# Kernel tuning notes

Hardware: AMD Instinct MI355X
Metric: run time of the kernel (lower is better)

Reference implementation:

```python
import jax, jax.numpy as jnp
import numpy as np
import math

HIDDEN = 128   # hidden_size (per-head dim) used for 1/sqrt(d) scaling
SPAN = 1024    # attn_span
B, M = 32, 1024
K_LEN = M + SPAN


def _unskew(X, span):
    """X: [B, M, K] -> [B, M, span], out[b,m,l] = X[b, m, m+l].
    Equivalent to the torch pad/view/slice trick (shift row m left by m)."""
    _, Mq, _ = X.shape
    rows = jnp.arange(Mq)[:, None]                 # [M,1]
    cols = rows + jnp.arange(span)[None, :]        # [M,span]
    return X[:, rows, cols]


def _skew(X, pad_value):
    """X: [B, M, L] -> [B, M, M+L], out[b,m,j] = X[b,m,j-m] if 0<=j-m<L else pad.
    Equivalent to the torch pad/view/slice trick (shift row m right by m)."""
    _, Mq, L = X.shape
    m = jnp.arange(Mq)[:, None]                    # [M,1]
    rel = jnp.arange(Mq + L)[None, :] - m          # [M, M+L]
    valid = (rel >= 0) & (rel < L)
    gathered = X[:, m, jnp.clip(rel, 0, L - 1)]    # [B, M, M+L]
    return jnp.where(valid, gathered, pad_value)


def setup_inputs() -> dict:
    key = jax.random.key(0)
    k1, k2, k3, k4 = jax.random.split(key, 4)
    return {
        "query": jax.random.normal(k1, (B, M, HIDDEN), dtype=jnp.float32),
        "key": jax.random.normal(k2, (B, K_LEN, HIDDEN), dtype=jnp.float32),
        "value": jax.random.normal(k3, (B, K_LEN, HIDDEN), dtype=jnp.float32),
        "pos_encoding": jax.random.normal(k4, (HIDDEN, SPAN), dtype=jnp.float32),
    }


def reference(query, key, value, pos_encoding):
    span = pos_encoding.shape[-1]
    # context scores: [B, M, M+span]
    attn_ctx = jnp.einsum('bmh,bkh->bmk', query, key)
    attn_ctx = _unskew(attn_ctx, span)             # [B, M, span]
    # relative-position scores: [B, M, span]
    attn_pos = jnp.einsum('bmh,hl->bml', query, pos_encoding)
    attn = (attn_ctx + attn_pos) / math.sqrt(HIDDEN)
    attn = jax.nn.softmax(attn, axis=-1)           # dropout p=0 -> identity
    attn_sk = _skew(attn, 0.0)                     # [B, M, M+span]
    return jnp.einsum('bmk,bkh->bmh', attn_sk, value)
```

## Files before the change

kernel.cpp:

```cpp
#include <hip/hip_runtime.h>
#include <hip/hip_bf16.h>

#define B_    32
#define M_    1024
#define H_    128
#define SPAN_ 1024
#define KL_   2048
#define NITER 17
#define SCALE 0.08838834764831845f

typedef __attribute__((ext_vector_type(8))) short bf16x8;
typedef __attribute__((ext_vector_type(4))) float f32x4;

#define WSNEED 262144ull

static __device__ __forceinline__ unsigned int cvt_pk2(float lo, float hi) {
  unsigned int r;
  asm("v_cvt_pk_bf16_f32 %0, %1, %2" : "=v"(r) : "v"(lo), "v"(hi));
  return r;
}
static __device__ __forceinline__ unsigned short f2b(float x) {
  unsigned int u = __builtin_bit_cast(unsigned int, x);
  return (unsigned short)((u + 0x7FFFu + ((u >> 16) & 1u)) >> 16);
}
static __device__ __forceinline__ float b2f(unsigned short u) {
  return __builtin_bit_cast(float, ((unsigned int)u) << 16);
}
static __device__ __forceinline__ bf16x8 ldfrag(const char* p) {
  short4 a = *(const short4*)p;
  short4 b = *(const short4*)(p + 8);
  bf16x8 r;
  r[0] = a.x; r[1] = a.y; r[2] = a.z; r[3] = a.w;
  r[4] = b.x; r[5] = b.y; r[6] = b.z; r[7] = b.w;
  return r;
}

__global__ void __launch_bounds__(256) convP2(const float* __restrict__ pe,
                                              char* __restrict__ out) {
  __shared__ float tile[128 * 66];
  int lt = blockIdx.x, tid = threadIdx.x;
#pragma unroll
  for (int i = 0; i < 8; ++i) {
    int idx = i * 256 + tid;
    int h = idx >> 4, c4 = idx & 15;
    float4 x = *(const float4*)(pe + (size_t)h * 1024 + lt * 64 + c4 * 4);
    tile[h * 66 + c4 * 4 + 0] = x.x; tile[h * 66 + c4 * 4 + 1] = x.y;
    tile[h * 66 + c4 * 4 + 2] = x.z; tile[h * 66 + c4 * 4 + 3] = x.w;
  }
  __syncthreads();
  char* dst = out + (size_t)lt * 16384;
#pragma unroll
  for (int j = 0; j < 4; ++j) {
    int u = tid >> 4;
    int l = (tid & 15) + 16 * j;
    uint4 d;
    d.x = cvt_pk2(tile[(8 * u + 0) * 66 + l], tile[(8 * u + 1) * 66 + l]);
    d.y = cvt_pk2(tile[(8 * u + 2) * 66 + l], tile[(8 * u + 3) * 66 + l]);
    d.z = cvt_pk2(tile[(8 * u + 4) * 66 + l], tile[(8 * u + 5) * 66 + l]);
    d.w = cvt_pk2(tile[(8 * u + 6) * 66 + l], tile[(8 * u + 7) * 66 + l]);
    *(uint4*)(dst + l * 256 + 16 * u) = d;
  }
}

#define PITCH_A  264
#define PITCH_VT 136
#define PITCH_PR 264
#define PITCH_PW 136
#define OFF_K  0
#define OFF_VT 16896
#define OFF_PT 34304
#define OFF_PR 51200
#define OFF_PW 68096
#define LDS_FB 76800

__global__ void __launch_bounds__(256, 2) seqattn_main(
    const float* __restrict__ q, const float* __restrict__ kkey,
    const float* __restrict__ vval, const char* __restrict__ posws,
    float* __restrict__ out) {
  extern __shared__ char smem[];
  char* KL = smem + OFF_K;
  char* VT = smem + OFF_VT;
  char* PT = smem + OFF_PT;
  char* PR = smem + OFF_PR;
  char* PW = smem + OFF_PW;

  int jb = blockIdx.x;
  int o  = (jb & 7) * 64 + (jb >> 3);
  int b  = o >> 4;
  int m0 = (o & 15) * 64;

  int tid  = threadIdx.x;
  int w    = tid >> 6;
  int lane = tid & 63;
  int g    = lane >> 4;
  int c    = lane & 15;
  int r0   = tid >> 5;
  int c4   = tid & 31;

  const float* qbase = q    + ((size_t)b * M_  + m0) * H_;
  const float* kbase = kkey + ((size_t)b * KL_ + m0) * H_;
  const float* vbase = vval + ((size_t)b * KL_ + m0) * H_;

  float4 kpre[8];
  float  vpre[32];
  uint4  ppre[4];

#define LOADK(tt) do {                                                        \
    const float* kb_ = kbase + (size_t)(64 * (tt)) * H_;                      \
    _Pragma("unroll")                                                         \
    for (int p = 0; p < 8; ++p)                                               \
      kpre[p] = *(const float4*)(kb_ + (p * 8 + r0) * H_ + c4 * 4);           \
  } while (0)
#define WRITEK() do {                                                         \
    _Pragma("unroll")                                                         \
    for (int p = 0; p < 8; ++p) {                                             \
      float4 v_ = kpre[p];                                                    \
      uint2 d_; d_.x = cvt_pk2(v_.x, v_.y); d_.y = cvt_pk2(v_.z, v_.w);       \
      *(uint2*)(KL + (p * 8 + r0) * PITCH_A + c4 * 8) = d_;                   \
    }                                                                         \
  } while (0)
#define LOADV(tt) do {                                                        \
    const float* vb_ = vbase + (size_t)(64 * (tt)) * H_;                      \
    _Pragma("unroll")                                                         \
    for (int qq = 0; qq < 4; ++qq) {                                          \
      int kq_ = 4 * (4 * w + qq);                                             \
      _Pragma("unroll")                                                       \
      for (int r = 0; r < 4; ++r) {                                           \
        vpre[qq * 8 + r * 2 + 0] = vb_[(kq_ + r) * H_ + lane];                \
        vpre[qq * 8 + r * 2 + 1] = vb_[(kq_ + r) * H_ + lane + 64];           \
      }                                                                       \
    }                                                                         \
  } while (0)
#define WRITEV() do {                                                         \
    _Pragma("unroll")                                                         \
    for (int qq = 0; qq < 4; ++qq) {                                          \
      int kq_ = 4 * w + qq;                                                   \
      uint2 lo_, hi_;                                                         \
      lo_.x = cvt_pk2(vpre[qq * 8 + 0], vpre[qq * 8 + 2]);                    \
      lo_.y = cvt_pk2(vpre[qq * 8 + 4], vpre[qq * 8 + 6]);                    \
      hi_.x = cvt_pk2(vpre[qq * 8 + 1], vpre[qq * 8 + 3]);                    \
      hi_.y = cvt_pk2(vpre[qq * 8 + 5], vpre[qq * 8 + 7]);                    \
      *(uint2*)(VT + lane * PITCH_VT + 8 * kq_) = lo_;                        \
      *(uint2*)(VT + (lane + 64) * PITCH_VT + 8 * kq_) = hi_;                 \
    }                                                                         \
  } while (0)
#define LOADP2(tt) do {                                                       \
    const char* pt_ = posws + (size_t)(tt) * 16384;                           \
    _Pragma("unroll")                                                         \
    for (int i = 0; i < 4; ++i)                                               \
      ppre[i] = *(const uint4*)(pt_ + (i * 256 + tid) * 16);                  \
  } while (0)
#define WRITEP2() do {                                                        \
    _Pragma("unroll")                                                         \
    for (int i = 0; i < 4; ++i) {                                             \
      int idx_ = i * 256 + tid;                                               \
      int pr_ = idx_ >> 4, pu_ = idx_ & 15;                                   \
      uint2 lo_, hi_;                                                         \
      lo_.x = ppre[i].x; lo_.y = ppre[i].y;                                   \
      hi_.x = ppre[i].z; hi_.y = ppre[i].w;                                   \
      *(uint2*)(PT + pr_ * PITCH_A + pu_ * 16) = lo_;                         \
      *(uint2*)(PT + pr_ * PITCH_A + pu_ * 16 + 8) = hi_;                     \
    }                                                                         \
  } while (0)

  {
    float4 qpre[8];
#pragma unroll
    for (int p = 0; p < 8; ++p)
      qpre[p] = *(const float4*)(qbase + (p * 8 + r0) * H_ + c4 * 4);
    LOADK(0); LOADV(0); LOADP2(0);
#pragma unroll
    for (int p = 0; p < 8; ++p) {
      float4 v_ = qpre[p];
      uint2 d_;
      d_.x = cvt_pk2(v_.x * SCALE, v_.y * SCALE);
      d_.y = cvt_pk2(v_.z * SCALE, v_.w * SCALE);
      *(uint2*)(PR + (p * 8 + r0) * PITCH_PR + c4 * 8) = d_;
    }
    WRITEK(); WRITEV(); WRITEP2();
    LOADK(1); LOADV(1); LOADP2(1);
  }
  __syncthreads();

  bf16x8 qf[4];
#pragma unroll
  for (int hs = 0; hs < 4; ++hs)
    qf[hs] = ldfrag(PR + (w * 16 + c) * PITCH_PR + hs * 64 + g * 16);

  f32x4 O[8];
#pragma unroll
  for (int i = 0; i < 8; ++i) { O[i][0] = 0.f; O[i][1] = 0.f; O[i][2] = 0.f; O[i][3] = 0.f; }
  float mrun = -1e30f, lrun = 0.f;
  const int mrow = 16 * w + c;
  char* prRow = PR + mrow * PITCH_PR;
  char* pwRow = PW + mrow * PITCH_PW;

#pragma unroll 1
  for (int t = 0; t < NITER; ++t) {
    if (t < 16) {
      __builtin_amdgcn_s_setprio(1);
#pragma unroll
      for (int lt = 0; lt < 4; ++lt) {
        f32x4 pb = {0.f, 0.f, 0.f, 0.f};
#pragma unroll
        for (int hs = 0; hs < 4; ++hs)
          pb = __builtin_amdgcn_mfma_f32_16x16x32_bf16(
              ldfrag(PT + (16 * lt + c) * PITCH_A + hs * 64 + g * 16), qf[hs], pb, 0, 0, 0);
#pragma unroll
        for (int rr = 0; rr < 4; ++rr) {
          int x = (64 * t + 16 * lt + 4 * g + rr + mrow) & 127;
          *(unsigned short*)(prRow + x * 2) = f2b(pb[rr]);
        }
      }
      __builtin_amdgcn_s_setprio(0);
    }
    f32x4 s[4];
    __builtin_amdgcn_s_setprio(1);
#pragma unroll
    for (int nt = 0; nt < 4; ++nt) {
      f32x4 acc = {0.f, 0.f, 0.f, 0.f};
#pragma unroll
      for (int hs = 0; hs < 4; ++hs)
        acc = __builtin_amdgcn_mfma_f32_16x16x32_bf16(
            ldfrag(KL + (16 * nt + c) * PITCH_A + hs * 64 + g * 16), qf[hs], acc, 0, 0, 0);
      s[nt] = acc;
    }
    __builtin_amdgcn_s_setprio(0);
#pragma unroll
    for (int nt = 0; nt < 4; ++nt) {
      int x = (64 * t + 16 * nt + 4 * g) & 127;
      ushort4 bv = *(const ushort4*)(prRow + x * 2);
      int lbase = 64 * t + 16 * nt + 4 * g - mrow;
      const unsigned short* bp = (const unsigned short*)&bv;
#pragma unroll
      for (int rr = 0; rr < 4; ++rr) {
        float sv = s[nt][rr] + b2f(bp[rr]);
        s[nt][rr] = ((unsigned)(lbase + rr) < 1024u) ? sv : -1e30f;
      }
    }
    float pmax = -1e30f;
#pragma unroll
    for (int nt = 0; nt < 4; ++nt)
#pragma unroll
      for (int rr = 0; rr < 4; ++rr) pmax = fmaxf(pmax, s[nt][rr]);
    pmax = fmaxf(pmax, __shfl_xor(pmax, 16, 64));
    pmax = fmaxf(pmax, __shfl_xor(pmax, 32, 64));
    if (__any(pmax > mrun + 8.0f)) {
      float mn = fmaxf(mrun, pmax);
      float corr = __expf(mrun - mn);
      mrun = mn;
      lrun *= corr;
#pragma unroll
      for (int i = 0; i < 8; ++i) {
        O[i][0] *= corr; O[i][1] *= corr; O[i][2] *= corr; O[i][3] *= corr;
      }
    }
    float rsum = 0.f;
#pragma unroll
    for (int nt = 0; nt < 4; ++nt) {
      float p0 = __expf(s[nt][0] - mrun);
      float p1 = __expf(s[nt][1] - mrun);
      float p2 = __expf(s[nt][2] - mrun);
      float p3 = __expf(s[nt][3] - mrun);
      rsum += (p0 + p1) + (p2 + p3);
      uint2 d_;
      d_.x = cvt_pk2(p0, p1);
      d_.y = cvt_pk2(p2, p3);
      *(uint2*)(pwRow + (16 * nt + 4 * g) * 2) = d_;
    }
    rsum += __shfl_xor(rsum, 16, 64);
    rsum += __shfl_xor(rsum, 32, 64);
    lrun += rsum;
    __builtin_amdgcn_s_setprio(1);
#pragma unroll
    for (int ks = 0; ks < 2; ++ks) {
      bf16x8 pfrag = ldfrag(pwRow + ks * 64 + g * 16);
#pragma unroll
      for (int nt = 0; nt < 8; ++nt)
        O[nt] = __builtin_amdgcn_mfma_f32_16x16x32_bf16(
            ldfrag(VT + (16 * nt + c) * PITCH_VT + ks * 64 + g * 16), pfrag, O[nt], 0, 0, 0);
    }
    __builtin_amdgcn_s_setprio(0);
    __syncthreads();
    if (t < 16) {
      WRITEK(); WRITEV();
      if (t < 15) {
        WRITEP2();
        LOADK(t + 2); LOADV(t + 2);
        if (t + 2 < 16) LOADP2(t + 2);
      }
    }
    __syncthreads();
  }

  float inv = 1.0f / lrun;
  float* ob = out + ((size_t)b * M_ + m0 + mrow) * H_;
#pragma unroll
  for (int nt = 0; nt < 8; ++nt) {
    float4 vv;
    vv.x = O[nt][0] * inv; vv.y = O[nt][1] * inv;
    vv.z = O[nt][2] * inv; vv.w = O[nt][3] * inv;
    *(float4*)(ob + 16 * nt + 4 * g) = vv;
  }
}
#undef LOADK
#undef WRITEK
#undef LOADV
#undef WRITEV
#undef LOADP2
#undef WRITEP2

__global__ void __launch_bounds__(256, 2) seqattn_fb(
    const float* __restrict__ q, const float* __restrict__ kkey,
    const float* __restrict__ vval, const float* __restrict__ pe,
    float* __restrict__ out) {
  extern __shared__ char smem[];
  char* KL = smem + OFF_K;
  char* VT = smem + OFF_VT;
  char* PT = smem + OFF_PT;
  char* PR = smem + OFF_PR;
  char* PW = smem + OFF_PW;

  int jb = blockIdx.x;
  int o  = (jb & 7) * 64 + (jb >> 3);
  int b  = o >> 4;
  int m0 = (o & 15) * 64;

  int tid  = threadIdx.x;
  int w    = tid >> 6;
  int lane = tid & 63;
  int g    = lane >> 4;
  int c    = lane & 15;
  int r0   = tid >> 5;
  int c4   = tid & 31;

  const float* qbase = q    + ((size_t)b * M_  + m0) * H_;
  const float* kbase = kkey + ((size_t)b * KL_ + m0) * H_;
  const float* vbase = vval + ((size_t)b * KL_ + m0) * H_;

  float4 kpre[8];
  float  vpre[32];
  float  ppre[32];

#define LOADK(tt) do {                                                        \
    const float* kb_ = kbase + (size_t)(64 * (tt)) * H_;                      \
    _Pragma("unroll")                                                         \
    for (int p = 0; p < 8; ++p)                                               \
      kpre[p] = *(const float4*)(kb_ + (p * 8 + r0) * H_ + c4 * 4);           \
  } while (0)
#define WRITEK() do {                                                         \
    _Pragma("unroll")                                                         \
    for (int p = 0; p < 8; ++p) {                                             \
      float4 v_ = kpre[p];                                                    \
      uint2 d_; d_.x = cvt_pk2(v_.x, v_.y); d_.y = cvt_pk2(v_.z, v_.w);       \
      *(uint2*)(KL + (p * 8 + r0) * PITCH_A + c4 * 8) = d_;                   \
    }                                                                         \
  } while (0)
#define LOADV(tt) do {                                                        \
    const float* vb_ = vbase + (size_t)(64 * (tt)) * H_;                      \
    _Pragma("unroll")                                                         \
    for (int qq = 0; qq < 4; ++qq) {                                          \
      int kq_ = 4 * (4 * w + qq);                                             \
      _Pragma("unroll")                                                       \
      for (int r = 0; r < 4; ++r) {                                           \
        vpre[qq * 8 + r * 2 + 0] = vb_[(kq_ + r) * H_ + lane];                \
        vpre[qq * 8 + r * 2 + 1] = vb_[(kq_ + r) * H_ + lane + 64];           \
      }                                                                       \
    }                                                                         \
  } while (0)
#define WRITEV() do {                                                         \
    _Pragma("unroll")                                                         \
    for (int qq = 0; qq < 4; ++qq) {                                          \
      int kq_ = 4 * w + qq;                                                   \
      uint2 lo_, hi_;                                                         \
      lo_.x = cvt_pk2(vpre[qq * 8 + 0], vpre[qq * 8 + 2]);                    \
      lo_.y = cvt_pk2(vpre[qq * 8 + 4], vpre[qq * 8 + 6]);                    \
      hi_.x = cvt_pk2(vpre[qq * 8 + 1], vpre[qq * 8 + 3]);                    \
      hi_.y = cvt_pk2(vpre[qq * 8 + 5], vpre[qq * 8 + 7]);                    \
      *(uint2*)(VT + lane * PITCH_VT + 8 * kq_) = lo_;                        \
      *(uint2*)(VT + (lane + 64) * PITCH_VT + 8 * kq_) = hi_;                 \
    }                                                                         \
  } while (0)
#define LOADP(tt) do {                                                        \
    const float* pb_ = pe + 64 * (tt);                                        \
    _Pragma("unroll")                                                         \
    for (int qq = 0; qq < 8; ++qq) {                                          \
      int h_ = 4 * (8 * w + qq);                                              \
      _Pragma("unroll")                                                       \
      for (int r = 0; r < 4; ++r)                                             \
        ppre[qq * 4 + r] = pb_[(h_ + r) * SPAN_ + lane];                      \
    }                                                                         \
  } while (0)
#define WRITEP() do {                                                         \
    _Pragma("unroll")                                                         \
    for (int qq = 0; qq < 8; ++qq) {                                          \
      uint2 d_;                                                               \
      d_.x = cvt_pk2(ppre[qq * 4 + 0], ppre[qq * 4 + 1]);                     \
      d_.y = cvt_pk2(ppre[qq * 4 + 2], ppre[qq * 4 + 3]);                     \
      *(uint2*)(PT + lane * PITCH_A + 8 * (8 * w + qq)) = d_;                 \
    }                                                                         \
  } while (0)

  {
    float4 qpre[8];
#pragma unroll
    for (int p = 0; p < 8; ++p)
      qpre[p] = *(const float4*)(qbase + (p * 8 + r0) * H_ + c4 * 4);
    LOADK(0); LOADV(0); LOADP(0);
#pragma unroll
    for (int p = 0; p < 8; ++p) {
      float4 v_ = qpre[p];
      uint2 d_;
      d_.x = cvt_pk2(v_.x * SCALE, v_.y * SCALE);
      d_.y = cvt_pk2(v_.z * SCALE, v_.w * SCALE);
      *(uint2*)(PR + (p * 8 + r0) * PITCH_PR + c4 * 8) = d_;
    }
    WRITEK(); WRITEV(); WRITEP();
    LOADK(1); LOADV(1); LOADP(1);
  }
  __syncthreads();

  bf16x8 qf[4];
#pragma unroll
  for (int hs = 0; hs < 4; ++hs)
    qf[hs] = ldfrag(PR + (w * 16 + c) * PITCH_PR + hs * 64 + g * 16);

  f32x4 O[8];
#pragma unroll
  for (int i = 0; i < 8; ++i) { O[i][0] = 0.f; O[i][1] = 0.f; O[i][2] = 0.f; O[i][3] = 0.f; }
  float mrun = -1e30f, lrun = 0.f;
  const int mrow = 16 * w + c;
  char* prRow = PR + mrow * PITCH_PR;
  char* pwRow = PW + mrow * PITCH_PW;

#pragma unroll 1
  for (int t = 0; t < NITER; ++t) {
    if (t < 16) {
#pragma unroll
      for (int lt = 0; lt < 4; ++lt) {
        f32x4 pb = {0.f, 0.f, 0.f, 0.f};
#pragma unroll
        for (int hs = 0; hs < 4; ++hs)
          pb = __builtin_amdgcn_mfma_f32_16x16x32_bf16(
              ldfrag(PT + (16 * lt + c) * PITCH_A + hs * 64 + g * 16), qf[hs], pb, 0, 0, 0);
#pragma unroll
        for (int rr = 0; rr < 4; ++rr) {
          int x = (64 * t + 16 * lt + 4 * g + rr + mrow) & 127;
          *(unsigned short*)(prRow + x * 2) = f2b(pb[rr]);
        }
      }
    }
    f32x4 s[4];
#pragma unroll
    for (int nt = 0; nt < 4; ++nt) {
      f32x4 acc = {0.f, 0.f, 0.f, 0.f};
#pragma unroll
      for (int hs = 0; hs < 4; ++hs)
        acc = __builtin_amdgcn_mfma_f32_16x16x32_bf16(
            ldfrag(KL + (16 * nt + c) * PITCH_A + hs * 64 + g * 16), qf[hs], acc, 0, 0, 0);
      s[nt] = acc;
    }
#pragma unroll
    for (int nt = 0; nt < 4; ++nt) {
      int x = (64 * t + 16 * nt + 4 * g) & 127;
      ushort4 bv = *(const ushort4*)(prRow + x * 2);
      int lbase = 64 * t + 16 * nt + 4 * g - mrow;
      const unsigned short* bp = (const unsigned short*)&bv;
#pragma unroll
      for (int rr = 0; rr < 4; ++rr) {
        float sv = s[nt][rr] + b2f(bp[rr]);
        s[nt][rr] = ((unsigned)(lbase + rr) < 1024u) ? sv : -1e30f;
      }
    }
    float pmax = -1e30f;
#pragma unroll
    for (int nt = 0; nt < 4; ++nt)
#pragma unroll
      for (int rr = 0; rr < 4; ++rr) pmax = fmaxf(pmax, s[nt][rr]);
    pmax = fmaxf(pmax, __shfl_xor(pmax, 16, 64));
    pmax = fmaxf(pmax, __shfl_xor(pmax, 32, 64));
    if (__any(pmax > mrun + 8.0f)) {
      float mn = fmaxf(mrun, pmax);
      float corr = __expf(mrun - mn);
      mrun = mn;
      lrun *= corr;
#pragma unroll
      for (int i = 0; i < 8; ++i) {
        O[i][0] *= corr; O[i][1] *= corr; O[i][2] *= corr; O[i][3] *= corr;
      }
    }
    float rsum = 0.f;
#pragma unroll
    for (int nt = 0; nt < 4; ++nt) {
      float p0 = __expf(s[nt][0] - mrun);
      float p1 = __expf(s[nt][1] - mrun);
      float p2 = __expf(s[nt][2] - mrun);
      float p3 = __expf(s[nt][3] - mrun);
      rsum += (p0 + p1) + (p2 + p3);
      uint2 d_;
      d_.x = cvt_pk2(p0, p1);
      d_.y = cvt_pk2(p2, p3);
      *(uint2*)(pwRow + (16 * nt + 4 * g) * 2) = d_;
    }
    rsum += __shfl_xor(rsum, 16, 64);
    rsum += __shfl_xor(rsum, 32, 64);
    lrun += rsum;
#pragma unroll
    for (int ks = 0; ks < 2; ++ks) {
      bf16x8 pfrag = ldfrag(pwRow + ks * 64 + g * 16);
#pragma unroll
      for (int nt = 0; nt < 8; ++nt)
        O[nt] = __builtin_amdgcn_mfma_f32_16x16x32_bf16(
            ldfrag(VT + (16 * nt + c) * PITCH_VT + ks * 64 + g * 16), pfrag, O[nt], 0, 0, 0);
    }
    __syncthreads();
    if (t < 16) {
      WRITEK(); WRITEV();
      if (t < 15) {
        WRITEP();
        LOADK(t + 2); LOADV(t + 2);
        if (t + 2 < 16) LOADP(t + 2);
      }
    }
    __syncthreads();
  }

  float inv = 1.0f / lrun;
  float* ob = out + ((size_t)b * M_ + m0 + mrow) * H_;
#pragma unroll
  for (int nt = 0; nt < 8; ++nt) {
    float4 vv;
    vv.x = O[nt][0] * inv; vv.y = O[nt][1] * inv;
    vv.z = O[nt][2] * inv; vv.w = O[nt][3] * inv;
    *(float4*)(ob + 16 * nt + 4 * g) = vv;
  }
}
#undef LOADK
#undef WRITEK
#undef LOADV
#undef WRITEV
#undef LOADP
#undef WRITEP

extern "C" void kernel_launch(void* const* d_in, const int* in_sizes, int n_in,
                              void* d_out, int out_size, void* d_ws, size_t ws_size,
                              hipStream_t stream) {
  const float* q  = (const float*)d_in[0];
  const float* k  = (const float*)d_in[1];
  const float* v  = (const float*)d_in[2];
  const float* pe = (const float*)d_in[3];
  float* out = (float*)d_out;

  if (ws_size >= WSNEED) {
    char* ws = (char*)d_ws;
    convP2<<<dim3(16), dim3(256), 0, stream>>>(pe, ws);
    (void)hipFuncSetAttribute(reinterpret_cast<const void*>(seqattn_main),
                              hipFuncAttributeMaxDynamicSharedMemorySize, LDS_FB);
    seqattn_main<<<dim3(512), dim3(256), LDS_FB, stream>>>(q, k, v, ws, out);
  } else {
    (void)hipFuncSetAttribute(reinterpret_cast<const void*>(seqattn_fb),
                              hipFuncAttributeMaxDynamicSharedMemorySize, LDS_FB);
    seqattn_fb<<<dim3(512), dim3(256), LDS_FB, stream>>>(q, k, v, pe, out);
  }
}
```

Before: 80.41 us.

## Warp-specialize attention kernel with producer waves and direct global-to-LDS pos loads

Restructures the main kernel into 512-thread blocks where four waves act as producers that load and convert K/V tiles to bf16 and stage the positional tile via global_load_lds, while four consumer waves run the MFMA score, softmax and PV work. The positional workspace is now written with an XOR swizzle, so the consumer reads it directly without padding. The aim is to overlap global loads with compute and take register pressure for prefetch buffers off the compute waves. The cost is extra waves per block, two barriers per iteration and a different LDS layout, which could limit occupancy.

```diff
diff --git a/kernel.cpp b/kernel.cpp
--- a/kernel.cpp
+++ b/kernel.cpp
@@ -33,6 +33,11 @@
   r[0] = a.x; r[1] = a.y; r[2] = a.z; r[3] = a.w;
   r[4] = b.x; r[5] = b.y; r[6] = b.z; r[7] = b.w;
   return r;
+}
+static __device__ __forceinline__ void gll16(char* lds, const char* g) {
+  __builtin_amdgcn_global_load_lds(
+      (const __attribute__((address_space(1))) unsigned int*)g,
+      (__attribute__((address_space(3))) unsigned int*)lds, 16, 0, 0);
 }
 
 __global__ void __launch_bounds__(256) convP2(const float* __restrict__ pe,
@@ -58,12 +63,256 @@
     d.y = cvt_pk2(tile[(8 * u + 2) * 66 + l], tile[(8 * u + 3) * 66 + l]);
     d.z = cvt_pk2(tile[(8 * u + 4) * 66 + l], tile[(8 * u + 5) * 66 + l]);
     d.w = cvt_pk2(tile[(8 * u + 6) * 66 + l], tile[(8 * u + 7) * 66 + l]);
-    *(uint4*)(dst + l * 256 + 16 * u) = d;
+    *(uint4*)(dst + l * 256 + 16 * (u ^ (l & 7))) = d;
   }
 }
 
 #define PITCH_A  264
 #define PITCH_VT 136
+#define MOFF_K  0
+#define MOFF_VT 16896
+#define MOFF_PT 34304
+#define MOFF_PR 50688
+#define MOFF_PW 67584
+#define LDS_MAIN 76288
+
+__global__ void __launch_bounds__(512, 4) seqattn_main(
+    const float* __restrict__ q, const float* __restrict__ kkey,
+    const float* __restrict__ vval, const char* __restrict__ posws,
+    float* __restrict__ out) {
+  extern __shared__ char smem[];
+  char* KL = smem + MOFF_K;
+  char* VT = smem + MOFF_VT;
+  char* PT = smem + MOFF_PT;
+  char* PR = smem + MOFF_PR;
+  char* PW = smem + MOFF_PW;
+
+  int jb = blockIdx.x;
+  int o  = (jb & 7) * 64 + (jb >> 3);
+  int b  = o >> 4;
+  int m0 = (o & 15) * 64;
+
+  int tid  = threadIdx.x;
+  bool isProd = tid >= 256;
+  int w    = tid >> 6;
+  int lane = tid & 63;
+  int g    = lane >> 4;
+  int c    = lane & 15;
+  int r0   = tid >> 5;
+  int c4   = tid & 31;
+  int sx   = c & 7;
+  int ptid  = tid & 255;
+  int pw    = ptid >> 6;
+  int plane = ptid & 63;
+  int pr0   = ptid >> 5;
+  int pc4   = ptid & 31;
+
+  const float* qbase = q    + ((size_t)b * M_  + m0) * H_;
+  const float* kbase = kkey + ((size_t)b * KL_ + m0) * H_;
+  const float* vbase = vval + ((size_t)b * KL_ + m0) * H_;
+
+  uint2 kbf[8];
+  uint2 vlo[4], vhi[4];
+
+#define PLOADK(tt) do {                                                       \
+    const float* kb_ = kbase + (size_t)(64 * (tt)) * H_;                      \
+    _Pragma("unroll")                                                         \
+    for (int p = 0; p < 8; ++p) {                                             \
+      float4 v_ = *(const float4*)(kb_ + (p * 8 + pr0) * H_ + pc4 * 4);       \
+      kbf[p].x = cvt_pk2(v_.x, v_.y);                                         \
+      kbf[p].y = cvt_pk2(v_.z, v_.w);                                         \
+    }                                                                         \
+  } while (0)
+#define PWRITEK() do {                                                        \
+    _Pragma("unroll")                                                         \
+    for (int p = 0; p < 8; ++p)                                               \
+      *(uint2*)(KL + (p * 8 + pr0) * PITCH_A + pc4 * 8) = kbf[p];             \
+  } while (0)
+#define PLOADV(tt) do {                                                       \
+    const float* vb_ = vbase + (size_t)(64 * (tt)) * H_;                      \
+    _Pragma("unroll")                                                         \
+    for (int qq = 0; qq < 4; ++qq) {                                          \
+      int kq_ = 4 * (4 * pw + qq);                                            \
+      float a0 = vb_[(kq_ + 0) * H_ + plane];                                 \
+      float a1 = vb_[(kq_ + 1) * H_ + plane];                                 \
+      float a2 = vb_[(kq_ + 2) * H_ + plane];                                 \
+      float a3 = vb_[(kq_ + 3) * H_ + plane];                                 \
+      float b0 = vb_[(kq_ + 0) * H_ + plane + 64];                            \
+      float b1 = vb_[(kq_ + 1) * H_ + plane + 64];                            \
+      float b2 = vb_[(kq_ + 2) * H_ + plane + 64];                            \
+      float b3 = vb_[(kq_ + 3) * H_ + plane + 64];                            \
+      vlo[qq].x = cvt_pk2(a0, a1); vlo[qq].y = cvt_pk2(a2, a3);               \
+      vhi[qq].x = cvt_pk2(b0, b1); vhi[qq].y = cvt_pk2(b2, b3);               \
+    }                                                                         \
+  } while (0)
+#define PWRITEV() do {                                                        \
+    _Pragma("unroll")                                                         \
+    for (int qq = 0; qq < 4; ++qq) {                                          \
+      int kq_ = 4 * pw + qq;                                                  \
+      *(uint2*)(VT + plane * PITCH_VT + 8 * kq_) = vlo[qq];                   \
+      *(uint2*)(VT + (plane + 64) * PITCH_VT + 8 * kq_) = vhi[qq];            \
+    }                                                                         \
+  } while (0)
+#define PSTAGEP(tt) do {                                                      \
+    const char* ps_ = posws + (size_t)(tt) * 16384;                           \
+    _Pragma("unroll")                                                         \
+    for (int i = 0; i < 4; ++i)                                               \
+      gll16(PT + (4 * pw + i) * 1024, ps_ + (4 * pw + i) * 1024 + plane * 16);\
+  } while (0)
+
+  if (!isProd) {
+    float4 qpre[8];
+#pragma unroll
+    for (int p = 0; p < 8; ++p)
+      qpre[p] = *(const float4*)(qbase + (p * 8 + r0) * H_ + c4 * 4);
+#pragma unroll
+    for (int p = 0; p < 8; ++p) {
+      float4 v_ = qpre[p];
+      uint2 d_;
+      d_.x = cvt_pk2(v_.x * SCALE, v_.y * SCALE);
+      d_.y = cvt_pk2(v_.z * SCALE, v_.w * SCALE);
+      *(uint2*)(PR + (p * 8 + r0) * PITCH_A + c4 * 8) = d_;
+    }
+  } else {
+    PLOADK(0); PLOADV(0);
+    PSTAGEP(0);
+    PWRITEK(); PWRITEV();
+  }
+  __syncthreads();
+
+  bf16x8 qf[4];
+  if (!isProd) {
+#pragma unroll
+    for (int hs = 0; hs < 4; ++hs)
+      qf[hs] = ldfrag(PR + (w * 16 + c) * PITCH_A + hs * 64 + g * 16);
+  }
+
+  f32x4 O[8];
+#pragma unroll
+  for (int i = 0; i < 8; ++i) { O[i][0] = 0.f; O[i][1] = 0.f; O[i][2] = 0.f; O[i][3] = 0.f; }
+  float mrun = -1e30f, lrun = 0.f;
+  const int mrow = 16 * w + c;
+  char* prRow = PR + mrow * PITCH_A;
+  char* pwRow = PW + mrow * PITCH_VT;
+
+#pragma unroll 1
+  for (int t = 0; t < NITER; ++t) {
+    if (!isProd) {
+      if (t < 16) {
+        __builtin_amdgcn_s_setprio(1);
+#pragma unroll
+        for (int lt = 0; lt < 4; ++lt) {
+          f32x4 pb = {0.f, 0.f, 0.f, 0.f};
+#pragma unroll
+          for (int hs = 0; hs < 4; ++hs) {
+            const char* pp = PT + (16 * lt + c) * 256 + 16 * (((hs << 2) | g) ^ sx);
+            pb = __builtin_amdgcn_mfma_f32_16x16x32_bf16(
+                *(const bf16x8*)pp, qf[hs], pb, 0, 0, 0);
+          }
+#pragma unroll
+          for (int rr = 0; rr < 4; ++rr) {
+            int x = (64 * t + 16 * lt + 4 * g + rr + mrow) & 127;
+            *(unsigned short*)(prRow + x * 2) = f2b(pb[rr]);
+          }
+        }
+        __builtin_amdgcn_s_setprio(0);
+      }
+      f32x4 s[4];
+      __builtin_amdgcn_s_setprio(1);
+#pragma unroll
+      for (int nt = 0; nt < 4; ++nt) {
+        f32x4 acc = {0.f, 0.f, 0.f, 0.f};
+#pragma unroll
+        for (int hs = 0; hs < 4; ++hs)
+          acc = __builtin_amdgcn_mfma_f32_16x16x32_bf16(
+              ldfrag(KL + (16 * nt + c) * PITCH_A + hs * 64 + g * 16), qf[hs], acc, 0, 0, 0);
+        s[nt] = acc;
+      }
+      __builtin_amdgcn_s_setprio(0);
+#pragma unroll
+      for (int nt = 0; nt < 4; ++nt) {
+        int x = (64 * t + 16 * nt + 4 * g) & 127;
+        ushort4 bv = *(const ushort4*)(prRow + x * 2);
+        int lbase = 64 * t + 16 * nt + 4 * g - mrow;
+        const unsigned short* bp = (const unsigned short*)&bv;
+#pragma unroll
+        for (int rr = 0; rr < 4; ++rr) {
+          float sv = s[nt][rr] + b2f(bp[rr]);
+          s[nt][rr] = ((unsigned)(lbase + rr) < 1024u) ? sv : -1e30f;
+        }
+      }
+      float pmax = -1e30f;
+#pragma unroll
+      for (int nt = 0; nt < 4; ++nt)
+#pragma unroll
+        for (int rr = 0; rr < 4; ++rr) pmax = fmaxf(pmax, s[nt][rr]);
+      pmax = fmaxf(pmax, __shfl_xor(pmax, 16, 64));
+      pmax = fmaxf(pmax, __shfl_xor(pmax, 32, 64));
+      if (__any(pmax > mrun + 8.0f)) {
+        float mn = fmaxf(mrun, pmax);
+        float corr = __expf(mrun - mn);
+        mrun = mn;
+        lrun *= corr;
+#pragma unroll
+        for (int i = 0; i < 8; ++i) {
+          O[i][0] *= corr; O[i][1] *= corr; O[i][2] *= corr; O[i][3] *= corr;
+        }
+      }
+      float rsum = 0.f;
+#pragma unroll
+      for (int nt = 0; nt < 4; ++nt) {
+        float p0 = __expf(s[nt][0] - mrun);
+        float p1 = __expf(s[nt][1] - mrun);
+        float p2 = __expf(s[nt][2] - mrun);
+        float p3 = __expf(s[nt][3] - mrun);
+        rsum += (p0 + p1) + (p2 + p3);
+        uint2 d_;
+        d_.x = cvt_pk2(p0, p1);
+        d_.y = cvt_pk2(p2, p3);
+        *(uint2*)(pwRow + (16 * nt + 4 * g) * 2) = d_;
+      }
+      rsum += __shfl_xor(rsum, 16, 64);
+      rsum += __shfl_xor(rsum, 32, 64);
+      lrun += rsum;
+      __builtin_amdgcn_s_setprio(1);
+#pragma unroll
+      for (int ks = 0; ks < 2; ++ks) {
+        bf16x8 pfrag = ldfrag(pwRow + ks * 64 + g * 16);
+#pragma unroll
+        for (int nt = 0; nt < 8; ++nt)
+          O[nt] = __builtin_amdgcn_mfma_f32_16x16x32_bf16(
+              ldfrag(VT + (16 * nt + c) * PITCH_VT + ks * 64 + g * 16), pfrag, O[nt], 0, 0, 0);
+      }
+      __builtin_amdgcn_s_setprio(0);
+    } else {
+      if (t < 16) { PLOADK(t + 1); PLOADV(t + 1); }
+    }
+    __syncthreads();
+    if (isProd && t < 16) {
+      PWRITEK(); PWRITEV();
+      if (t + 1 < 16) PSTAGEP(t + 1);
+    }
+    __syncthreads();
+  }
+
+  if (!isProd) {
+    float inv = 1.0f / lrun;
+    float* ob = out + ((size_t)b * M_ + m0 + mrow) * H_;
+#pragma unroll
+    for (int nt = 0; nt < 8; ++nt) {
+      float4 vv;
+      vv.x = O[nt][0] * inv; vv.y = O[nt][1] * inv;
+      vv.z = O[nt][2] * inv; vv.w = O[nt][3] * inv;
+      *(float4*)(ob + 16 * nt + 4 * g) = vv;
+    }
+  }
+}
+#undef PLOADK
+#undef PWRITEK
+#undef PLOADV
+#undef PWRITEV
+#undef PSTAGEP
+
 #define PITCH_PR 264
 #define PITCH_PW 136
 #define OFF_K  0
@@ -73,9 +322,9 @@
 #define OFF_PW 68096
 #define LDS_FB 76800
 
-__global__ void __launch_bounds__(256, 2) seqattn_main(
+__global__ void __launch_bounds__(256, 2) seqattn_fb(
     const float* __restrict__ q, const float* __restrict__ kkey,
-    const float* __restrict__ vval, const char* __restrict__ posws,
+    const float* __restrict__ vval, const float* __restrict__ pe,
     float* __restrict__ out) {
   extern __shared__ char smem[];
   char* KL = smem + OFF_K;
@@ -103,7 +352,7 @@
 
   float4 kpre[8];
   float  vpre[32];
-  uint4  ppre[4];
+  float  ppre[32];
 
 #define LOADK(tt) do {                                                        \
     const float* kb_ = kbase + (size_t)(64 * (tt)) * H_;                      \
@@ -144,22 +393,23 @@
       *(uint2*)(VT + (lane + 64) * PITCH_VT + 8 * kq_) = hi_;                 \
     }                                                                         \
   } while (0)
-#define LOADP2(tt) do {                                                       \
-    const char* pt_ = posws + (size_t)(tt) * 16384;                           \
-    _Pragma("unroll")                                                         \
-    for (int i = 0; i < 4; ++i)                                               \
-      ppre[i] = *(const uint4*)(pt_ + (i * 256 + tid) * 16);                  \
-  } while (0)
-#define WRITEP2() do {                                                        \
-    _Pragma("unroll")                                                         \
-    for (int i = 0; i < 4; ++i) {                                             \
-      int idx_ = i * 256 + tid;                                               \
-      int pr_ = idx_ >> 4, pu_ = idx_ & 15;                                   \
-      uint2 lo_, hi_;                                                         \
-      lo_.x = ppre[i].x; lo_.y = ppre[i].y;                                   \
-      hi_.x = ppre[i].z; hi_.y = ppre[i].w;                                   \
-      *(uint2*)(PT + pr_ * PITCH_A + pu_ * 16) = lo_;                         \
-      *(uint2*)(PT + pr_ * PITCH_A + pu_ * 16 + 8) = hi_;                     \
+#define LOADP(tt) do {                                                        \
+    const float* pb_ = pe + 64 * (tt);                                        \
+    _Pragma("unroll")                                                         \
+    for (int qq = 0; qq < 8; ++qq) {                                          \
+      int h_ = 4 * (8 * w + qq);                                              \
+      _Pragma("unroll")                                                       \
+      for (int r = 0; r < 4; ++r)                                             \
+        ppre[qq * 4 + r] = pb_[(h_ + r) * SPAN_ + lane];                      \
+    }                                                                         \
+  } while (0)
+#define WRITEP() do {                                                         \
+    _Pragma("unroll")                                                         \
+    for (int qq = 0; qq < 8; ++qq) {                                          \
+      uint2 d_;                                                               \
+      d_.x = cvt_pk2(ppre[qq * 4 + 0], ppre[qq * 4 + 1]);                     \
+      d_.y = cvt_pk2(ppre[qq * 4 + 2], ppre[qq * 4 + 3]);                     \
+      *(uint2*)(PT + lane * PITCH_A + 8 * (8 * w + qq)) = d_;                 \
     }                                                                         \
   } while (0)
 
@@ -168,7 +418,7 @@
 #pragma unroll
     for (int p = 0; p < 8; ++p)
       qpre[p] = *(const float4*)(qbase + (p * 8 + r0) * H_ + c4 * 4);
-    LOADK(0); LOADV(0); LOADP2(0);
+    LOADK(0); LOADV(0); LOADP(0);
 #pragma unroll
     for (int p = 0; p < 8; ++p) {
       float4 v_ = qpre[p];
@@ -177,8 +427,8 @@
       d_.y = cvt_pk2(v_.z * SCALE, v_.w * SCALE);
       *(uint2*)(PR + (p * 8 + r0) * PITCH_PR + c4 * 8) = d_;
     }
-    WRITEK(); WRITEV(); WRITEP2();
-    LOADK(1); LOADV(1); LOADP2(1);
+    WRITEK(); WRITEV(); WRITEP();
+    LOADK(1); LOADV(1); LOADP(1);
   }
   __syncthreads();
 
@@ -198,7 +448,6 @@
 #pragma unroll 1
   for (int t = 0; t < NITER; ++t) {
     if (t < 16) {
-      __builtin_amdgcn_s_setprio(1);
 #pragma unroll
       for (int lt = 0; lt < 4; ++lt) {
         f32x4 pb = {0.f, 0.f, 0.f, 0.f};
@@ -212,10 +461,8 @@
           *(unsigned short*)(prRow + x * 2) = f2b(pb[rr]);
         }
       }
-      __builtin_amdgcn_s_setprio(0);
     }
     f32x4 s[4];
-    __builtin_amdgcn_s_setprio(1);
 #pragma unroll
     for (int nt = 0; nt < 4; ++nt) {
       f32x4 acc = {0.f, 0.f, 0.f, 0.f};
@@ -225,7 +472,6 @@
             ldfrag(KL + (16 * nt + c) * PITCH_A + hs * 64 + g * 16), qf[hs], acc, 0, 0, 0);
       s[nt] = acc;
     }
-    __builtin_amdgcn_s_setprio(0);
 #pragma unroll
     for (int nt = 0; nt < 4; ++nt) {
       int x = (64 * t + 16 * nt + 4 * g) & 127;
@@ -271,240 +517,6 @@
     rsum += __shfl_xor(rsum, 16, 64);
     rsum += __shfl_xor(rsum, 32, 64);
     lrun += rsum;
-    __builtin_amdgcn_s_setprio(1);
-#pragma unroll
-    for (int ks = 0; ks < 2; ++ks) {
-      bf16x8 pfrag = ldfrag(pwRow + ks * 64 + g * 16);
-#pragma unroll
-      for (int nt = 0; nt < 8; ++nt)
-        O[nt] = __builtin_amdgcn_mfma_f32_16x16x32_bf16(
-            ldfrag(VT + (16 * nt + c) * PITCH_VT + ks * 64 + g * 16), pfrag, O[nt], 0, 0, 0);
-    }
-    __builtin_amdgcn_s_setprio(0);
-    __syncthreads();
-    if (t < 16) {
-      WRITEK(); WRITEV();
-      if (t < 15) {
-        WRITEP2();
-        LOADK(t + 2); LOADV(t + 2);
-        if (t + 2 < 16) LOADP2(t + 2);
-      }
-    }
-    __syncthreads();
-  }
-
-  float inv = 1.0f / lrun;
-  float* ob = out + ((size_t)b * M_ + m0 + mrow) * H_;
-#pragma unroll
-  for (int nt = 0; nt < 8; ++nt) {
-    float4 vv;
-    vv.x = O[nt][0] * inv; vv.y = O[nt][1] * inv;
-    vv.z = O[nt][2] * inv; vv.w = O[nt][3] * inv;
-    *(float4*)(ob + 16 * nt + 4 * g) = vv;
-  }
-}
-#undef LOADK
-#undef WRITEK
-#undef LOADV
-#undef WRITEV
-#undef LOADP2
-#undef WRITEP2
-
-__global__ void __launch_bounds__(256, 2) seqattn_fb(
-    const float* __restrict__ q, const float* __restrict__ kkey,
-    const float* __restrict__ vval, const float* __restrict__ pe,
-    float* __restrict__ out) {
-  extern __shared__ char smem[];
-  char* KL = smem + OFF_K;
-  char* VT = smem + OFF_VT;
-  char* PT = smem + OFF_PT;
-  char* PR = smem + OFF_PR;
-  char* PW = smem + OFF_PW;
-
-  int jb = blockIdx.x;
-  int o  = (jb & 7) * 64 + (jb >> 3);
-  int b  = o >> 4;
-  int m0 = (o & 15) * 64;
-
-  int tid  = threadIdx.x;
-  int w    = tid >> 6;
-  int lane = tid & 63;
-  int g    = lane >> 4;
-  int c    = lane & 15;
-  int r0   = tid >> 5;
-  int c4   = tid & 31;
-
-  const float* qbase = q    + ((size_t)b * M_  + m0) * H_;
-  const float* kbase = kkey + ((size_t)b * KL_ + m0) * H_;
-  const float* vbase = vval + ((size_t)b * KL_ + m0) * H_;
-
-  float4 kpre[8];
-  float  vpre[32];
-  float  ppre[32];
-
-#define LOADK(tt) do {                                                        \
-    const float* kb_ = kbase + (size_t)(64 * (tt)) * H_;                      \
-    _Pragma("unroll")                                                         \
-    for (int p = 0; p < 8; ++p)                                               \
-      kpre[p] = *(const float4*)(kb_ + (p * 8 + r0) * H_ + c4 * 4);           \
-  } while (0)
-#define WRITEK() do {                                                         \
-    _Pragma("unroll")                                                         \
-    for (int p = 0; p < 8; ++p) {                                             \
-      float4 v_ = kpre[p];                                                    \
-      uint2 d_; d_.x = cvt_pk2(v_.x, v_.y); d_.y = cvt_pk2(v_.z, v_.w);       \
-      *(uint2*)(KL + (p * 8 + r0) * PITCH_A + c4 * 8) = d_;                   \
-    }                                                                         \
-  } while (0)
-#define LOADV(tt) do {                                                        \
-    const float* vb_ = vbase + (size_t)(64 * (tt)) * H_;                      \
-    _Pragma("unroll")                                                         \
-    for (int qq = 0; qq < 4; ++qq) {                                          \
-      int kq_ = 4 * (4 * w + qq);                                             \
-      _Pragma("unroll")                                                       \
-      for (int r = 0; r < 4; ++r) {                                           \
-        vpre[qq * 8 + r * 2 + 0] = vb_[(kq_ + r) * H_ + lane];                \
-        vpre[qq * 8 + r * 2 + 1] = vb_[(kq_ + r) * H_ + lane + 64];           \
-      }                                                                       \
-    }                                                                         \
-  } while (0)
-#define WRITEV() do {                                                         \
-    _Pragma("unroll")                                                         \
-    for (int qq = 0; qq < 4; ++qq) {                                          \
-      int kq_ = 4 * w + qq;                                                   \
-      uint2 lo_, hi_;                                                         \
-      lo_.x = cvt_pk2(vpre[qq * 8 + 0], vpre[qq * 8 + 2]);                    \
-      lo_.y = cvt_pk2(vpre[qq * 8 + 4], vpre[qq * 8 + 6]);                    \
-      hi_.x = cvt_pk2(vpre[qq * 8 + 1], vpre[qq * 8 + 3]);                    \
-      hi_.y = cvt_pk2(vpre[qq * 8 + 5], vpre[qq * 8 + 7]);                    \
-      *(uint2*)(VT + lane * PITCH_VT + 8 * kq_) = lo_;                        \
-      *(uint2*)(VT + (lane + 64) * PITCH_VT + 8 * kq_) = hi_;                 \
-    }                                                                         \
-  } while (0)
-#define LOADP(tt) do {                                                        \
-    const float* pb_ = pe + 64 * (tt);                                        \
-    _Pragma("unroll")                                                         \
-    for (int qq = 0; qq < 8; ++qq) {                                          \
-      int h_ = 4 * (8 * w + qq);                                              \
-      _Pragma("unroll")                                                       \
-      for (int r = 0; r < 4; ++r)                                             \
-        ppre[qq * 4 + r] = pb_[(h_ + r) * SPAN_ + lane];                      \
-    }                                                                         \
-  } while (0)
-#define WRITEP() do {                                                         \
-    _Pragma("unroll")                                                         \
-    for (int qq = 0; qq < 8; ++qq) {                                          \
-      uint2 d_;                                                               \
-      d_.x = cvt_pk2(ppre[qq * 4 + 0], ppre[qq * 4 + 1]);                     \
-      d_.y = cvt_pk2(ppre[qq * 4 + 2], ppre[qq * 4 + 3]);                     \
-      *(uint2*)(PT + lane * PITCH_A + 8 * (8 * w + qq)) = d_;                 \
-    }                                                                         \
-  } while (0)
-
-  {
-    float4 qpre[8];
-#pragma unroll
-    for (int p = 0; p < 8; ++p)
-      qpre[p] = *(const float4*)(qbase + (p * 8 + r0) * H_ + c4 * 4);
-    LOADK(0); LOADV(0); LOADP(0);
-#pragma unroll
-    for (int p = 0; p < 8; ++p) {
-      float4 v_ = qpre[p];
-      uint2 d_;
-      d_.x = cvt_pk2(v_.x * SCALE, v_.y * SCALE);
-      d_.y = cvt_pk2(v_.z * SCALE, v_.w * SCALE);
-      *(uint2*)(PR + (p * 8 + r0) * PITCH_PR + c4 * 8) = d_;
-    }
-    WRITEK(); WRITEV(); WRITEP();
-    LOADK(1); LOADV(1); LOADP(1);
-  }
-  __syncthreads();
-
-  bf16x8 qf[4];
-#pragma unroll
-  for (int hs = 0; hs < 4; ++hs)
-    qf[hs] = ldfrag(PR + (w * 16 + c) * PITCH_PR + hs * 64 + g * 16);
-
-  f32x4 O[8];
-#pragma unroll
-  for (int i = 0; i < 8; ++i) { O[i][0] = 0.f; O[i][1] = 0.f; O[i][2] = 0.f; O[i][3] = 0.f; }
-  float mrun = -1e30f, lrun = 0.f;
-  const int mrow = 16 * w + c;
-  char* prRow = PR + mrow * PITCH_PR;
-  char* pwRow = PW + mrow * PITCH_PW;
-
-#pragma unroll 1
-  for (int t = 0; t < NITER; ++t) {
-    if (t < 16) {
-#pragma unroll
-      for (int lt = 0; lt < 4; ++lt) {
-        f32x4 pb = {0.f, 0.f, 0.f, 0.f};
-#pragma unroll
-        for (int hs = 0; hs < 4; ++hs)
-          pb = __builtin_amdgcn_mfma_f32_16x16x32_bf16(
-              ldfrag(PT + (16 * lt + c) * PITCH_A + hs * 64 + g * 16), qf[hs], pb, 0, 0, 0);
-#pragma unroll
-        for (int rr = 0; rr < 4; ++rr) {
-          int x = (64 * t + 16 * lt + 4 * g + rr + mrow) & 127;
-          *(unsigned short*)(prRow + x * 2) = f2b(pb[rr]);
-        }
-      }
-    }
-    f32x4 s[4];
-#pragma unroll
-    for (int nt = 0; nt < 4; ++nt) {
-      f32x4 acc = {0.f, 0.f, 0.f, 0.f};
-#pragma unroll
-      for (int hs = 0; hs < 4; ++hs)
-        acc = __builtin_amdgcn_mfma_f32_16x16x32_bf16(
-            ldfrag(KL + (16 * nt + c) * PITCH_A + hs * 64 + g * 16), qf[hs], acc, 0, 0, 0);
-      s[nt] = acc;
-    }
-#pragma unroll
-    for (int nt = 0; nt < 4; ++nt) {
-      int x = (64 * t + 16 * nt + 4 * g) & 127;
-      ushort4 bv = *(const ushort4*)(prRow + x * 2);
-      int lbase = 64 * t + 16 * nt + 4 * g - mrow;
-      const unsigned short* bp = (const unsigned short*)&bv;
-#pragma unroll
-      for (int rr = 0; rr < 4; ++rr) {
-        float sv = s[nt][rr] + b2f(bp[rr]);
-        s[nt][rr] = ((unsigned)(lbase + rr) < 1024u) ? sv : -1e30f;
-      }
-    }
-    float pmax = -1e30f;
-#pragma unroll
-    for (int nt = 0; nt < 4; ++nt)
-#pragma unroll
-      for (int rr = 0; rr < 4; ++rr) pmax = fmaxf(pmax, s[nt][rr]);
-    pmax = fmaxf(pmax, __shfl_xor(pmax, 16, 64));
-    pmax = fmaxf(pmax, __shfl_xor(pmax, 32, 64));
-    if (__any(pmax > mrun + 8.0f)) {
-      float mn = fmaxf(mrun, pmax);
-      float corr = __expf(mrun - mn);
-      mrun = mn;
-      lrun *= corr;
-#pragma unroll
-      for (int i = 0; i < 8; ++i) {
-        O[i][0] *= corr; O[i][1] *= corr; O[i][2] *= corr; O[i][3] *= corr;
-      }
-    }
-    float rsum = 0.f;
-#pragma unroll
-    for (int nt = 0; nt < 4; ++nt) {
-      float p0 = __expf(s[nt][0] - mrun);
-      float p1 = __expf(s[nt][1] - mrun);
-      float p2 = __expf(s[nt][2] - mrun);
-      float p3 = __expf(s[nt][3] - mrun);
-      rsum += (p0 + p1) + (p2 + p3);
-      uint2 d_;
-      d_.x = cvt_pk2(p0, p1);
-      d_.y = cvt_pk2(p2, p3);
-      *(uint2*)(pwRow + (16 * nt + 4 * g) * 2) = d_;
-    }
-    rsum += __shfl_xor(rsum, 16, 64);
-    rsum += __shfl_xor(rsum, 32, 64);
-    lrun += rsum;
 #pragma unroll
     for (int ks = 0; ks < 2; ++ks) {
       bf16x8 pfrag = ldfrag(pwRow + ks * 64 + g * 16);
@@ -555,8 +567,8 @@
     char* ws = (char*)d_ws;
     convP2<<<dim3(16), dim3(256), 0, stream>>>(pe, ws);
     (void)hipFuncSetAttribute(reinterpret_cast<const void*>(seqattn_main),
-                              hipFuncAttributeMaxDynamicSharedMemorySize, LDS_FB);
-    seqattn_main<<<dim3(512), dim3(256), LDS_FB, stream>>>(q, k, v, ws, out);
+                              hipFuncAttributeMaxDynamicSharedMemorySize, LDS_MAIN);
+    seqattn_main<<<dim3(512), dim3(512), LDS_MAIN, stream>>>(q, k, v, ws, out);
   } else {
     (void)hipFuncSetAttribute(reinterpret_cast<const void*>(seqattn_fb),
                               hipFuncAttributeMaxDynamicSharedMemorySize, LDS_FB);
```

Measured after the change: 142.0 us. +76.6%, slower.
